# Kernel tuning notes

Hardware: AMD Instinct MI355X
Metric: run time of the kernel (lower is better)

Reference implementation:

```python
import jax, jax.numpy as jnp
import numpy as np

K_HEADS = 8
D_HEAD = 16
D_MODEL = K_HEADS * D_HEAD  # 128
NEG_INF = -65504.0


def setup_inputs() -> dict:
    key = jax.random.key(0)
    ks = jax.random.split(key, 12)
    B, P, N, F = 8, 128, 256, D_MODEL
    Din = F + D_MODEL  # concat(X, STE) feature dim = 256
    g = lambda k, shape: (jax.random.normal(k, shape, dtype=jnp.float32)
                          * (1.0 / np.sqrt(shape[0])))
    inp = {
        "X": jax.random.normal(ks[0], (B, P, N, F), dtype=jnp.float32),
        "STE": jax.random.normal(ks[1], (B, P, N, D_MODEL), dtype=jnp.float32),
        "Wq": g(ks[2], (Din, D_MODEL)), "bq": jnp.zeros((D_MODEL,), jnp.float32),
        "Wk": g(ks[3], (Din, D_MODEL)), "bk": jnp.zeros((D_MODEL,), jnp.float32),
        "Wv": g(ks[4], (Din, D_MODEL)), "bv": jnp.zeros((D_MODEL,), jnp.float32),
        "W1": g(ks[5], (D_MODEL, D_MODEL)), "b1": jnp.zeros((D_MODEL,), jnp.float32),
        "W2": g(ks[6], (D_MODEL, D_MODEL)), "b2": jnp.zeros((D_MODEL,), jnp.float32),
    }
    return inp


def reference(X, STE, Wq, bq, Wk, bk, Wv, bv, W1, b1, W2, b2):
    B, P, N, _ = X.shape
    Kh, dh = K_HEADS, D_HEAD
    x_ = jnp.concatenate([X, STE], axis=-1)  # (B,P,N,2D)
    # FC layers are 1x1 convs == dense on last axis, activation relu
    q = jax.nn.relu(x_ @ Wq + bq)  # (B,P,N,D)
    k = jax.nn.relu(x_ @ Wk + bk)
    v = jax.nn.relu(x_ @ Wv + bv)
    # split heads: (B,P,N,K,d)
    q = q.reshape(B, P, N, Kh, dh)
    k = k.reshape(B, P, N, Kh, dh)
    v = v.reshape(B, P, N, Kh, dh)
    # scores over time axis per (batch, head, node): (B,K,N,P,P)
    scores = jnp.einsum("bpnkd,bqnkd->bknpq", q, k) / jnp.sqrt(
        jnp.asarray(dh, q.dtype))
    # causal lower-triangular mask over time
    tril = jnp.tril(jnp.ones((P, P), dtype=scores.dtype))
    scores = scores * tril + (1.0 - tril) * NEG_INF
    weights = jax.nn.softmax(scores, axis=-1)
    attended = jnp.einsum("bknpq,bqnkd->bpnkd", weights, v)  # (B,P,N,K,d)
    out = attended.reshape(B, P, N, Kh * dh)
    # output FC: [D relu, D none]
    out = jax.nn.relu(out @ W1 + b1)
    out = out @ W2 + b2
    return out
```

## Files before the change

### kernel.cpp

```cpp
#include <hip/hip_runtime.h>
#include <hip/hip_bf16.h>

#define PP     128
#define NNODE  256
#define DMODEL 128
#define DIN    256
#define LSTR   136
#define NEGINF -65504.0f

typedef __attribute__((ext_vector_type(4))) float          f32x4;
typedef __attribute__((ext_vector_type(8))) __bf16         bf16x8;
typedef __attribute__((ext_vector_type(8))) unsigned short u16x8;

static __device__ __forceinline__ unsigned short f2b(float f) {
  union { float f; unsigned u; } x; x.f = f;
  unsigned r = x.u + 0x7fffu + ((x.u >> 16) & 1u);
  return (unsigned short)(r >> 16);
}

static __device__ __forceinline__ f32x4 zero4() {
  f32x4 v = {0.f, 0.f, 0.f, 0.f};
  return v;
}

static __device__ __forceinline__ bf16x8 zero_bf8() {
  u16x8 v = {0, 0, 0, 0, 0, 0, 0, 0};
  return __builtin_bit_cast(bf16x8, v);
}

static __device__ __forceinline__ bf16x8 ld_bf8(const unsigned short* p) {
  u16x8 v = *(const u16x8*)p;
  return __builtin_bit_cast(bf16x8, v);
}

static __device__ __forceinline__ f32x4 mfma16(bf16x8 a, bf16x8 b, f32x4 c) {
  return __builtin_amdgcn_mfma_f32_16x16x32_bf16(a, b, c, 0, 0, 0);
}

__global__ void prep_weights(const float* __restrict__ Wq, const float* __restrict__ Wk,
                             const float* __restrict__ Wv, const float* __restrict__ W1,
                             const float* __restrict__ W2, unsigned short* __restrict__ ws) {
  int idx = blockIdx.x * blockDim.x + threadIdx.x;
  if (idx < 98304) {
    int seg = idx >> 15;
    int r   = idx & 32767;
    int n   = r >> 8;
    int k   = r & 255;
    const float* W = (seg == 0) ? Wq : (seg == 1) ? Wk : Wv;
    ws[idx] = f2b(W[k * DMODEL + n]);
  } else if (idx < 131072) {
    int r   = idx - 98304;
    int seg = r >> 14;
    int rr  = r & 16383;
    int n   = rr >> 7;
    int k   = rr & 127;
    const float* W = (seg == 0) ? W1 : W2;
    ws[idx] = f2b(W[k * DMODEL + n]);
  }
}

__global__ __launch_bounds__(512, 2) void fused_attn(
    const float* __restrict__ X, const float* __restrict__ STE,
    const unsigned short* __restrict__ Wt,
    const float* __restrict__ bq, const float* __restrict__ bk,
    const float* __restrict__ bv, const float* __restrict__ b1,
    const float* __restrict__ b2, float* __restrict__ out) {
  __shared__ __align__(16) unsigned short s_x[PP * LSTR];
  __shared__ __align__(16) unsigned short s_q[PP * LSTR];
  __shared__ __align__(16) unsigned short s_k[PP * LSTR];
  __shared__ __align__(16) unsigned short s_v[PP * LSTR];

  const unsigned short* WqT = Wt;
  const unsigned short* WkT = Wt + 32768;
  const unsigned short* WvT = Wt + 65536;
  const unsigned short* W1T = Wt + 98304;
  const unsigned short* W2T = Wt + 114688;

  const int bid  = blockIdx.x;
  const int bb   = bid >> 8;
  const int nn   = bid & 255;
  const int tid  = threadIdx.x;
  const int wv   = tid >> 6;
  const int lane = tid & 63;
  const int quad = lane >> 4;
  const int l16  = lane & 15;
  const int mrow  = wv * 16 + l16;
  const int crow0 = wv * 16 + quad * 4;

  f32x4 accQ[8], accK[8], accV[8];
#pragma unroll
  for (int i = 0; i < 8; ++i) { accQ[i] = zero4(); accK[i] = zero4(); accV[i] = zero4(); }

  for (int chunk = 0; chunk < 2; ++chunk) {
    const float* src = chunk ? STE : X;
    {
      const int r0 = tid >> 5;
      const int c4 = (tid & 31) << 2;
#pragma unroll
      for (int it = 0; it < 8; ++it) {
        const int row = it * 16 + r0;
        const float4 v =
            *(const float4*)(src + (size_t)((bb * PP + row) * NNODE + nn) * DMODEL + c4);
        unsigned short* d = &s_x[row * LSTR + c4];
        d[0] = f2b(v.x); d[1] = f2b(v.y); d[2] = f2b(v.z); d[3] = f2b(v.w);
      }
    }
    __syncthreads();

    bf16x8 af[4];
#pragma unroll
    for (int ks = 0; ks < 4; ++ks)
      af[ks] = ld_bf8(&s_x[mrow * LSTR + ks * 32 + quad * 8]);

#pragma unroll
    for (int m = 0; m < 3; ++m) {
      const unsigned short* W =
          ((m == 0) ? WqT : (m == 1) ? WkT : WvT) + chunk * 128 + quad * 8;
      f32x4* acc = (m == 0) ? accQ : (m == 1) ? accK : accV;
#pragma unroll
      for (int ct = 0; ct < 8; ++ct) {
        const unsigned short* wr = W + (ct * 16 + l16) * DIN;
#pragma unroll
        for (int ks = 0; ks < 4; ++ks)
          acc[ct] = mfma16(af[ks], ld_bf8(wr + ks * 32), acc[ct]);
      }
    }
    __syncthreads();
  }

#pragma unroll
  for (int m = 0; m < 3; ++m) {
    const float* bias = (m == 0) ? bq : (m == 1) ? bk : bv;
    f32x4* acc = (m == 0) ? accQ : (m == 1) ? accK : accV;
#pragma unroll
    for (int ct = 0; ct < 8; ++ct) {
      const int col = ct * 16 + l16;
      const float bsc = bias[col];
#pragma unroll
      for (int r = 0; r < 4; ++r) {
        float v = acc[ct][r] + bsc;
        v = v > 0.f ? v : 0.f;
        const unsigned short h = f2b(v);
        const int row = crow0 + r;
        if (m == 0)      s_q[row * LSTR + col] = h;
        else if (m == 1) s_k[row * LSTR + col] = h;
        else             s_v[col * LSTR + row] = h;
      }
    }
  }
  __syncthreads();

  f32x4 attA[8];
#pragma unroll
  for (int i = 0; i < 8; ++i) attA[i] = zero4();

  for (int h = 0; h < 8; ++h) {
    bf16x8 aq = (quad < 2) ? ld_bf8(&s_q[mrow * LSTR + h * 16 + quad * 8]) : zero_bf8();
    f32x4 s[8];
#pragma unroll
    for (int ct = 0; ct < 8; ++ct) {
      bf16x8 bk8 =
          (quad < 2) ? ld_bf8(&s_k[(ct * 16 + l16) * LSTR + h * 16 + quad * 8]) : zero_bf8();
      s[ct] = mfma16(aq, bk8, zero4());
    }
#pragma unroll
    for (int r = 0; r < 4; ++r) {
      const int prow = crow0 + r;
      float mx = NEGINF;
#pragma unroll
      for (int ct = 0; ct < 8; ++ct) {
        const int cq = ct * 16 + l16;
        float v = s[ct][r] * 0.25f;
        v = (cq <= prow) ? v : NEGINF;
        s[ct][r] = v;
        mx = fmaxf(mx, v);
      }
#pragma unroll
      for (int off = 1; off < 16; off <<= 1) mx = fmaxf(mx, __shfl_xor(mx, off, 64));
      float sum = 0.f;
#pragma unroll
      for (int ct = 0; ct < 8; ++ct) {
        float e = __expf(s[ct][r] - mx);
        s[ct][r] = e;
        sum += e;
      }
#pragma unroll
      for (int off = 1; off < 16; off <<= 1) sum += __shfl_xor(sum, off, 64);
      const float inv = 1.0f / sum;
#pragma unroll
      for (int ct = 0; ct < 8; ++ct) s[ct][r] *= inv;
    }
    __syncthreads();
#pragma unroll
    for (int ct = 0; ct < 8; ++ct) {
      const int cq = ct * 16 + l16;
#pragma unroll
      for (int r = 0; r < 4; ++r)
        s_x[(crow0 + r) * LSTR + cq] = f2b(s[ct][r]);
    }
    __syncthreads();
#pragma unroll
    for (int ks = 0; ks < 4; ++ks) {
      bf16x8 ap  = ld_bf8(&s_x[mrow * LSTR + ks * 32 + quad * 8]);
      bf16x8 bv8 = ld_bf8(&s_v[(h * 16 + l16) * LSTR + ks * 32 + quad * 8]);
      attA[h] = mfma16(ap, bv8, attA[h]);
    }
  }
  __syncthreads();

#pragma unroll
  for (int h = 0; h < 8; ++h) {
    const int col = h * 16 + l16;
#pragma unroll
    for (int r = 0; r < 4; ++r)
      s_x[(crow0 + r) * LSTR + col] = f2b(attA[h][r]);
  }
  __syncthreads();

  f32x4 acc1[8];
#pragma unroll
  for (int i = 0; i < 8; ++i) acc1[i] = zero4();
  {
    bf16x8 af[4];
#pragma unroll
    for (int ks = 0; ks < 4; ++ks)
      af[ks] = ld_bf8(&s_x[mrow * LSTR + ks * 32 + quad * 8]);
#pragma unroll
    for (int ct = 0; ct < 8; ++ct) {
      const unsigned short* wr = W1T + (ct * 16 + l16) * DMODEL + quad * 8;
#pragma unroll
      for (int ks = 0; ks < 4; ++ks)
        acc1[ct] = mfma16(af[ks], ld_bf8(wr + ks * 32), acc1[ct]);
    }
  }
#pragma unroll
  for (int ct = 0; ct < 8; ++ct) {
    const int col = ct * 16 + l16;
    const float bsc = b1[col];
#pragma unroll
    for (int r = 0; r < 4; ++r) {
      float v = acc1[ct][r] + bsc;
      v = v > 0.f ? v : 0.f;
      s_k[(crow0 + r) * LSTR + col] = f2b(v);
    }
  }
  __syncthreads();

  f32x4 acc2[8];
#pragma unroll
  for (int i = 0; i < 8; ++i) acc2[i] = zero4();
  {
    bf16x8 af[4];
#pragma unroll
    for (int ks = 0; ks < 4; ++ks)
      af[ks] = ld_bf8(&s_k[mrow * LSTR + ks * 32 + quad * 8]);
#pragma unroll
    for (int ct = 0; ct < 8; ++ct) {
      const unsigned short* wr = W2T + (ct * 16 + l16) * DMODEL + quad * 8;
#pragma unroll
      for (int ks = 0; ks < 4; ++ks)
        acc2[ct] = mfma16(af[ks], ld_bf8(wr + ks * 32), acc2[ct]);
    }
  }
#pragma unroll
  for (int ct = 0; ct < 8; ++ct) {
    const int col = ct * 16 + l16;
    const float bsc = b2[col];
#pragma unroll
    for (int r = 0; r < 4; ++r) {
      const int row = crow0 + r;
      out[(size_t)((bb * PP + row) * NNODE + nn) * DMODEL + col] = acc2[ct][r] + bsc;
    }
  }
}

extern "C" void kernel_launch(void* const* d_in, const int* in_sizes, int n_in,
                              void* d_out, int out_size, void* d_ws, size_t ws_size,
                              hipStream_t stream) {
  const float* X   = (const float*)d_in[0];
  const float* STE = (const float*)d_in[1];
  const float* Wq  = (const float*)d_in[2];
  const float* bq  = (const float*)d_in[3];
  const float* Wk  = (const float*)d_in[4];
  const float* bk  = (const float*)d_in[5];
  const float* Wv  = (const float*)d_in[6];
  const float* bv  = (const float*)d_in[7];
  const float* W1  = (const float*)d_in[8];
  const float* b1  = (const float*)d_in[9];
  const float* W2  = (const float*)d_in[10];
  const float* b2  = (const float*)d_in[11];
  float* out = (float*)d_out;
  unsigned short* ws = (unsigned short*)d_ws;

  prep_weights<<<512, 256, 0, stream>>>(Wq, Wk, Wv, W1, W2, ws);
  fused_attn<<<2048, 512, 0, stream>>>(X, STE, ws, bq, bk, bv, b1, b2, out);
}
```

Baseline: 1.008 ms.

## Split fused kernel into QKV GEMM and attention+MLP kernels via workspace

Splits the single fused kernel into two. The first computes the QKV projections, reading rows coalesced across contiguous nodes, and writes bf16 Q/K/V to workspace in a node-major layout. The second loads Q/K directly from global memory and transposes only V into LDS. In attention, each wave now owns one head and needs no block barriers inside the head loop, and both kernels use less LDS to allow higher occupancy. The cost is an extra global round trip for Q/K/V (bf16), possibly batched into multiple launches if the workspace is small.

```diff
diff --git a/kernel.cpp b/kernel.cpp
--- a/kernel.cpp
+++ b/kernel.cpp
@@ -5,8 +5,10 @@
 #define NNODE  256
 #define DMODEL 128
 #define DIN    256
-#define LSTR   136
 #define NEGINF -65504.0f
+
+#define WOFF 131072
+#define PB   4194304
 
 typedef __attribute__((ext_vector_type(4))) float          f32x4;
 typedef __attribute__((ext_vector_type(8))) __bf16         bf16x8;
@@ -17,22 +19,18 @@
   unsigned r = x.u + 0x7fffu + ((x.u >> 16) & 1u);
   return (unsigned short)(r >> 16);
 }
-
 static __device__ __forceinline__ f32x4 zero4() {
   f32x4 v = {0.f, 0.f, 0.f, 0.f};
   return v;
 }
-
 static __device__ __forceinline__ bf16x8 zero_bf8() {
   u16x8 v = {0, 0, 0, 0, 0, 0, 0, 0};
   return __builtin_bit_cast(bf16x8, v);
 }
-
 static __device__ __forceinline__ bf16x8 ld_bf8(const unsigned short* p) {
   u16x8 v = *(const u16x8*)p;
   return __builtin_bit_cast(bf16x8, v);
 }
-
 static __device__ __forceinline__ f32x4 mfma16(bf16x8 a, bf16x8 b, f32x4 c) {
   return __builtin_amdgcn_mfma_f32_16x16x32_bf16(a, b, c, 0, 0, 0);
 }
@@ -59,121 +57,135 @@
   }
 }
 
-__global__ __launch_bounds__(512, 2) void fused_attn(
+__global__ __launch_bounds__(512, 4) void qkv_gemm(
     const float* __restrict__ X, const float* __restrict__ STE,
     const unsigned short* __restrict__ Wt,
     const float* __restrict__ bq, const float* __restrict__ bk,
-    const float* __restrict__ bv, const float* __restrict__ b1,
-    const float* __restrict__ b2, float* __restrict__ out) {
-  __shared__ __align__(16) unsigned short s_x[PP * LSTR];
-  __shared__ __align__(16) unsigned short s_q[PP * LSTR];
-  __shared__ __align__(16) unsigned short s_k[PP * LSTR];
-  __shared__ __align__(16) unsigned short s_v[PP * LSTR];
-
-  const unsigned short* WqT = Wt;
-  const unsigned short* WkT = Wt + 32768;
-  const unsigned short* WvT = Wt + 65536;
+    const float* __restrict__ bv,
+    unsigned short* __restrict__ q, unsigned short* __restrict__ k,
+    unsigned short* __restrict__ v, int b0) {
+  __shared__ __align__(16) unsigned short s_a[128 * 264];
+
+  const int R0 = blockIdx.x << 7;
+  const int n0 = R0 & 255;
+  const int p  = (R0 >> 8) & 127;
+  const int bl = R0 >> 15;
+  const int b  = b0 + bl;
+  const int tid = threadIdx.x;
+
+  {
+    const int row = tid >> 2;
+    const size_t rbase = (size_t)((b * PP + p) * NNODE + n0 + row) * DMODEL;
+    const float* xr = X + rbase;
+    const float* sr = STE + rbase;
+    unsigned short* d = &s_a[row * 264];
+#pragma unroll
+    for (int i = 0; i < 16; ++i) {
+      const int f = ((tid & 3) + i * 4) << 2;
+      const float4 vv = (f < 128) ? *(const float4*)(xr + f)
+                                  : *(const float4*)(sr + f - 128);
+      d[f] = f2b(vv.x); d[f + 1] = f2b(vv.y); d[f + 2] = f2b(vv.z); d[f + 3] = f2b(vv.w);
+    }
+  }
+  __syncthreads();
+
+  const int wv = tid >> 6, lane = tid & 63, quad = lane >> 4, l16 = lane & 15;
+  const int mrow = wv * 16 + l16, crow0 = wv * 16 + quad * 4;
+
+  bf16x8 af[8];
+#pragma unroll
+  for (int ks = 0; ks < 8; ++ks)
+    af[ks] = ld_bf8(&s_a[mrow * 264 + ks * 32 + quad * 8]);
+
+  for (int m = 0; m < 3; ++m) {
+    const unsigned short* W = Wt + m * 32768;
+    const float* bias = (m == 0) ? bq : (m == 1) ? bk : bv;
+    f32x4 acc[8];
+#pragma unroll
+    for (int i = 0; i < 8; ++i) acc[i] = zero4();
+#pragma unroll
+    for (int ct = 0; ct < 8; ++ct) {
+      const unsigned short* wr = W + (ct * 16 + l16) * DIN + quad * 8;
+#pragma unroll
+      for (int ks = 0; ks < 8; ++ks)
+        acc[ct] = mfma16(af[ks], ld_bf8(wr + ks * 32), acc[ct]);
+    }
+    unsigned short* outm = (m == 0) ? q : (m == 1) ? k : v;
+#pragma unroll
+    for (int ct = 0; ct < 8; ++ct) {
+      const int col = ct * 16 + l16;
+      const float bsc = bias[col];
+#pragma unroll
+      for (int r = 0; r < 4; ++r) {
+        float val = acc[ct][r] + bsc;
+        val = val > 0.f ? val : 0.f;
+        const int n = n0 + crow0 + r;
+        outm[((size_t)(bl * NNODE + n) * PP + p) * DMODEL + col] = f2b(val);
+      }
+    }
+  }
+}
+
+__global__ __launch_bounds__(512, 4) void attn_mlp(
+    const unsigned short* __restrict__ q, const unsigned short* __restrict__ k,
+    const unsigned short* __restrict__ v, const unsigned short* __restrict__ Wt,
+    const float* __restrict__ b1, const float* __restrict__ b2,
+    float* __restrict__ out, int b0) {
+  __shared__ __align__(16) unsigned short s_m[128 * 136];
+  __shared__ __align__(16) unsigned short s_n[128 * 136];
+
+  const int bid = blockIdx.x, bl = bid >> 8, nn = bid & 255;
+  const int bb = b0 + bl;
+  const int tid = threadIdx.x;
+  const int h = tid >> 6, lane = tid & 63, quad = lane >> 4, l16 = lane & 15;
+
+  const size_t slab = (size_t)(bl * NNODE + nn) * PP * DMODEL;
+  const unsigned short* qp = q + slab;
+  const unsigned short* kp = k + slab;
+  const unsigned short* vp = v + slab;
   const unsigned short* W1T = Wt + 98304;
   const unsigned short* W2T = Wt + 114688;
 
-  const int bid  = blockIdx.x;
-  const int bb   = bid >> 8;
-  const int nn   = bid & 255;
-  const int tid  = threadIdx.x;
-  const int wv   = tid >> 6;
-  const int lane = tid & 63;
-  const int quad = lane >> 4;
-  const int l16  = lane & 15;
-  const int mrow  = wv * 16 + l16;
-  const int crow0 = wv * 16 + quad * 4;
-
-  f32x4 accQ[8], accK[8], accV[8];
-#pragma unroll
-  for (int i = 0; i < 8; ++i) { accQ[i] = zero4(); accK[i] = zero4(); accV[i] = zero4(); }
-
-  for (int chunk = 0; chunk < 2; ++chunk) {
-    const float* src = chunk ? STE : X;
+  {
+    const int ph = lane >> 1, fh = lane & 1;
+#pragma unroll
+    for (int i = 0; i < 4; ++i) {
+      const int p = i * 32 + ph;
+      const u16x8 vv = *(const u16x8*)(vp + p * DMODEL + h * 16 + fh * 8);
+#pragma unroll
+      for (int j = 0; j < 8; ++j)
+        s_n[(h * 16 + fh * 8 + j) * 136 + p] = vv[j];
+    }
+  }
+
+  f32x4 att[8];
+#pragma unroll
+  for (int i = 0; i < 8; ++i) att[i] = zero4();
+
+  for (int mb = 0; mb < 8; ++mb) {
+    bf16x8 aq;
     {
-      const int r0 = tid >> 5;
-      const int c4 = (tid & 31) << 2;
-#pragma unroll
-      for (int it = 0; it < 8; ++it) {
-        const int row = it * 16 + r0;
-        const float4 v =
-            *(const float4*)(src + (size_t)((bb * PP + row) * NNODE + nn) * DMODEL + c4);
-        unsigned short* d = &s_x[row * LSTR + c4];
-        d[0] = f2b(v.x); d[1] = f2b(v.y); d[2] = f2b(v.z); d[3] = f2b(v.w);
-      }
-    }
-    __syncthreads();
-
-    bf16x8 af[4];
-#pragma unroll
-    for (int ks = 0; ks < 4; ++ks)
-      af[ks] = ld_bf8(&s_x[mrow * LSTR + ks * 32 + quad * 8]);
-
-#pragma unroll
-    for (int m = 0; m < 3; ++m) {
-      const unsigned short* W =
-          ((m == 0) ? WqT : (m == 1) ? WkT : WvT) + chunk * 128 + quad * 8;
-      f32x4* acc = (m == 0) ? accQ : (m == 1) ? accK : accV;
-#pragma unroll
-      for (int ct = 0; ct < 8; ++ct) {
-        const unsigned short* wr = W + (ct * 16 + l16) * DIN;
-#pragma unroll
-        for (int ks = 0; ks < 4; ++ks)
-          acc[ct] = mfma16(af[ks], ld_bf8(wr + ks * 32), acc[ct]);
-      }
-    }
-    __syncthreads();
-  }
-
-#pragma unroll
-  for (int m = 0; m < 3; ++m) {
-    const float* bias = (m == 0) ? bq : (m == 1) ? bk : bv;
-    f32x4* acc = (m == 0) ? accQ : (m == 1) ? accK : accV;
-#pragma unroll
-    for (int ct = 0; ct < 8; ++ct) {
-      const int col = ct * 16 + l16;
-      const float bsc = bias[col];
-#pragma unroll
-      for (int r = 0; r < 4; ++r) {
-        float v = acc[ct][r] + bsc;
-        v = v > 0.f ? v : 0.f;
-        const unsigned short h = f2b(v);
-        const int row = crow0 + r;
-        if (m == 0)      s_q[row * LSTR + col] = h;
-        else if (m == 1) s_k[row * LSTR + col] = h;
-        else             s_v[col * LSTR + row] = h;
-      }
-    }
-  }
-  __syncthreads();
-
-  f32x4 attA[8];
-#pragma unroll
-  for (int i = 0; i < 8; ++i) attA[i] = zero4();
-
-  for (int h = 0; h < 8; ++h) {
-    bf16x8 aq = (quad < 2) ? ld_bf8(&s_q[mrow * LSTR + h * 16 + quad * 8]) : zero_bf8();
+      bf16x8 t = ld_bf8(qp + (mb * 16 + l16) * DMODEL + h * 16 + (quad & 1) * 8);
+      aq = (quad < 2) ? t : zero_bf8();
+    }
     f32x4 s[8];
 #pragma unroll
     for (int ct = 0; ct < 8; ++ct) {
-      bf16x8 bk8 =
-          (quad < 2) ? ld_bf8(&s_k[(ct * 16 + l16) * LSTR + h * 16 + quad * 8]) : zero_bf8();
+      bf16x8 t = ld_bf8(kp + (ct * 16 + l16) * DMODEL + h * 16 + (quad & 1) * 8);
+      bf16x8 bk8 = (quad < 2) ? t : zero_bf8();
       s[ct] = mfma16(aq, bk8, zero4());
     }
 #pragma unroll
     for (int r = 0; r < 4; ++r) {
-      const int prow = crow0 + r;
+      const int prow = mb * 16 + quad * 4 + r;
       float mx = NEGINF;
 #pragma unroll
       for (int ct = 0; ct < 8; ++ct) {
         const int cq = ct * 16 + l16;
-        float v = s[ct][r] * 0.25f;
-        v = (cq <= prow) ? v : NEGINF;
-        s[ct][r] = v;
-        mx = fmaxf(mx, v);
+        float vv = s[ct][r] * 0.25f;
+        vv = (cq <= prow) ? vv : NEGINF;
+        s[ct][r] = vv;
+        mx = fmaxf(mx, vv);
       }
 #pragma unroll
       for (int off = 1; off < 16; off <<= 1) mx = fmaxf(mx, __shfl_xor(mx, off, 64));
@@ -190,47 +202,43 @@
 #pragma unroll
       for (int ct = 0; ct < 8; ++ct) s[ct][r] *= inv;
     }
-    __syncthreads();
-#pragma unroll
-    for (int ct = 0; ct < 8; ++ct) {
-      const int cq = ct * 16 + l16;
+#pragma unroll
+    for (int ct = 0; ct < 8; ++ct)
 #pragma unroll
       for (int r = 0; r < 4; ++r)
-        s_x[(crow0 + r) * LSTR + cq] = f2b(s[ct][r]);
-    }
-    __syncthreads();
+        s_m[(h * 16 + quad * 4 + r) * 136 + ct * 16 + l16] = f2b(s[ct][r]);
+    __asm__ volatile("s_waitcnt lgkmcnt(0)" ::: "memory");
 #pragma unroll
     for (int ks = 0; ks < 4; ++ks) {
-      bf16x8 ap  = ld_bf8(&s_x[mrow * LSTR + ks * 32 + quad * 8]);
-      bf16x8 bv8 = ld_bf8(&s_v[(h * 16 + l16) * LSTR + ks * 32 + quad * 8]);
-      attA[h] = mfma16(ap, bv8, attA[h]);
-    }
-  }
+      bf16x8 ap  = ld_bf8(&s_m[(h * 16 + l16) * 136 + ks * 32 + quad * 8]);
+      bf16x8 bv8 = ld_bf8(&s_n[(h * 16 + l16) * 136 + ks * 32 + quad * 8]);
+      att[mb] = mfma16(ap, bv8, att[mb]);
+    }
+  }
+
   __syncthreads();
-
-#pragma unroll
-  for (int h = 0; h < 8; ++h) {
-    const int col = h * 16 + l16;
+#pragma unroll
+  for (int mb = 0; mb < 8; ++mb)
 #pragma unroll
     for (int r = 0; r < 4; ++r)
-      s_x[(crow0 + r) * LSTR + col] = f2b(attA[h][r]);
-  }
+      s_m[(mb * 16 + quad * 4 + r) * 136 + h * 16 + l16] = f2b(att[mb][r]);
   __syncthreads();
 
+  const int crow0 = h * 16 + quad * 4;
   f32x4 acc1[8];
 #pragma unroll
   for (int i = 0; i < 8; ++i) acc1[i] = zero4();
   {
-    bf16x8 af[4];
+    bf16x8 a1[4];
 #pragma unroll
     for (int ks = 0; ks < 4; ++ks)
-      af[ks] = ld_bf8(&s_x[mrow * LSTR + ks * 32 + quad * 8]);
+      a1[ks] = ld_bf8(&s_m[(h * 16 + l16) * 136 + ks * 32 + quad * 8]);
 #pragma unroll
     for (int ct = 0; ct < 8; ++ct) {
       const unsigned short* wr = W1T + (ct * 16 + l16) * DMODEL + quad * 8;
 #pragma unroll
       for (int ks = 0; ks < 4; ++ks)
-        acc1[ct] = mfma16(af[ks], ld_bf8(wr + ks * 32), acc1[ct]);
+        acc1[ct] = mfma16(a1[ks], ld_bf8(wr + ks * 32), acc1[ct]);
     }
   }
 #pragma unroll
@@ -239,9 +247,9 @@
     const float bsc = b1[col];
 #pragma unroll
     for (int r = 0; r < 4; ++r) {
-      float v = acc1[ct][r] + bsc;
-      v = v > 0.f ? v : 0.f;
-      s_k[(crow0 + r) * LSTR + col] = f2b(v);
+      float vv = acc1[ct][r] + bsc;
+      vv = vv > 0.f ? vv : 0.f;
+      s_n[(crow0 + r) * 136 + col] = f2b(vv);
     }
   }
   __syncthreads();
@@ -250,16 +258,16 @@
 #pragma unroll
   for (int i = 0; i < 8; ++i) acc2[i] = zero4();
   {
-    bf16x8 af[4];
+    bf16x8 a2[4];
 #pragma unroll
     for (int ks = 0; ks < 4; ++ks)
-      af[ks] = ld_bf8(&s_k[mrow * LSTR + ks * 32 + quad * 8]);
+      a2[ks] = ld_bf8(&s_n[(h * 16 + l16) * 136 + ks * 32 + quad * 8]);
 #pragma unroll
     for (int ct = 0; ct < 8; ++ct) {
       const unsigned short* wr = W2T + (ct * 16 + l16) * DMODEL + quad * 8;
 #pragma unroll
       for (int ks = 0; ks < 4; ++ks)
-        acc2[ct] = mfma16(af[ks], ld_bf8(wr + ks * 32), acc2[ct]);
+        acc2[ct] = mfma16(a2[ks], ld_bf8(wr + ks * 32), acc2[ct]);
     }
   }
 #pragma unroll
@@ -293,5 +301,16 @@
   unsigned short* ws = (unsigned short*)d_ws;
 
   prep_weights<<<512, 256, 0, stream>>>(Wq, Wk, Wv, W1, W2, ws);
-  fused_attn<<<2048, 512, 0, stream>>>(X, STE, ws, bq, bk, bv, b1, b2, out);
-}
+
+  int nb = 8;
+  while (nb > 1 && 2ull * (WOFF + 3ull * nb * PB) > ws_size) nb >>= 1;
+
+  unsigned short* q = ws + WOFF;
+  unsigned short* kk = q + (size_t)nb * PB;
+  unsigned short* vv = kk + (size_t)nb * PB;
+
+  for (int b0 = 0; b0 < 8; b0 += nb) {
+    qkv_gemm<<<nb * 256, 512, 0, stream>>>(X, STE, ws, bq, bk, bv, q, kk, vv, b0);
+    attn_mlp<<<nb * 256, 512, 0, stream>>>(q, kk, vv, ws, b1, b2, out, b0);
+  }
+}
```

Measured after the change: 907.2 us. -10.0%, faster.
